# Performance work log

Measured on AMD Instinct MI355X. Metric: run time of the kernel, lower is better.

## Reference

```python
import jax, jax.numpy as jnp
import numpy as np

N_ITEMS = 1_000_000
N_FACTORS = 64

def setup_inputs() -> dict:
    key = jax.random.key(0)
    emb_weight = jax.random.normal(key, (N_ITEMS, N_FACTORS), dtype=jnp.float32)
    return {"emb_weight": emb_weight, "item_idx": 12345, "size": 50}

def reference(emb_weight, item_idx, size):
    # gather query row: u = emb(ind)  -> [d]
    u = emb_weight[item_idx]
    # scores = u @ emb.T  -> [n_items] (GEMV against full table)
    scores = emb_weight @ u
    # top-k retrieval (size <= n_items, clamp as in original)
    k = min(size, scores.shape[0])
    s, i = jax.lax.top_k(scores, k)
    return s, i
```

## Files before the change

### kernel.cpp

```cpp
#include <hip/hip_runtime.h>

#define NEG_INF (-1.0e30f)
#define CAP 4096
#define NBKT 4096

__device__ __forceinline__ unsigned flip(float f) {
    unsigned u = __float_as_uint(f);
    return (u & 0x80000000u) ? ~u : (u | 0x80000000u);
}

__device__ __forceinline__ bool pair_gt(float sa, int ia, float sb, int ib) {
    return (sa > sb) || (sa == sb && ia < ib);
}

__global__ __launch_bounds__(256) void k_gemv(const float* __restrict__ emb,
                                              const int* __restrict__ p_idx,
                                              float* __restrict__ scores) {
    const int tid   = threadIdx.x;
    const int col16 = tid & 15;
    const int grp   = tid >> 4;
    const float4 u4 = ((const float4*)(emb + (size_t)(*p_idx) * 64))[col16];
    const int base  = blockIdx.x * 64;
#pragma unroll
    for (int sub = 0; sub < 4; ++sub) {
        const int item = base + sub * 16 + grp;
        const float4 r = ((const float4*)(emb + (size_t)item * 64))[col16];
        float p = r.x * u4.x + r.y * u4.y + r.z * u4.z + r.w * u4.w;
        p += __shfl_xor(p, 1, 16);
        p += __shfl_xor(p, 2, 16);
        p += __shfl_xor(p, 4, 16);
        p += __shfl_xor(p, 8, 16);
        if (col16 == 0) scores[item] = p;
    }
}

__global__ __launch_bounds__(256) void k_hist(const float* __restrict__ scores,
                                              int n4, unsigned* __restrict__ hist) {
    __shared__ unsigned h[NBKT];
    const int tid = threadIdx.x;
    for (int i = tid; i < NBKT; i += 256) h[i] = 0;
    __syncthreads();
    const float4* s4 = (const float4*)scores;
    for (int i = blockIdx.x * 256 + tid; i < n4; i += gridDim.x * 256) {
        float4 v = s4[i];
        atomicAdd(&h[flip(v.x) >> 20], 1u);
        atomicAdd(&h[flip(v.y) >> 20], 1u);
        atomicAdd(&h[flip(v.z) >> 20], 1u);
        atomicAdd(&h[flip(v.w) >> 20], 1u);
    }
    __syncthreads();
    for (int i = tid; i < NBKT; i += 256) {
        unsigned c = h[i];
        if (c) atomicAdd(&hist[i], c);
    }
}

__global__ __launch_bounds__(256) void k_pick(const unsigned* __restrict__ hist,
                                              int k, unsigned* __restrict__ params) {
    __shared__ unsigned h[NBKT];
    __shared__ unsigned psum[256];
    const int tid = threadIdx.x;
    for (int i = tid; i < NBKT; i += 256) h[i] = hist[i];
    __syncthreads();
    const int base = tid * 16;
    unsigned local = 0;
#pragma unroll
    for (int j = 0; j < 16; ++j) local += h[base + j];
    psum[tid] = local;
    __syncthreads();
    for (int stride = 1; stride < 256; stride <<= 1) {
        unsigned add = (tid + stride < 256) ? psum[tid + stride] : 0u;
        __syncthreads();
        psum[tid] += add;
        __syncthreads();
    }
    unsigned c = (tid + 1 < 256) ? psum[tid + 1] : 0u;
    int found_b = -1; unsigned found_above = 0;
    for (int j = 15; j >= 0; --j) {
        unsigned hb = h[base + j];
        if (c < (unsigned)k && c + hb >= (unsigned)k) { found_b = base + j; found_above = c; }
        c += hb;
    }
    if (found_b >= 0) { params[0] = (unsigned)found_b; params[1] = found_above; }
}

__global__ __launch_bounds__(256) void k_compact(const float* __restrict__ scores,
                                                 int n4,
                                                 const unsigned* __restrict__ params,
                                                 unsigned* __restrict__ cnt,
                                                 float* __restrict__ cand_s,
                                                 int* __restrict__ cand_i) {
    const unsigned B = params[0];
    const float4* s4 = (const float4*)scores;
    for (int i = blockIdx.x * 256 + threadIdx.x; i < n4; i += gridDim.x * 256) {
        float4 v = s4[i];
        const float vv[4] = {v.x, v.y, v.z, v.w};
#pragma unroll
        for (int j = 0; j < 4; ++j) {
            if ((flip(vv[j]) >> 20) >= B) {
                unsigned pos = atomicAdd(cnt, 1u);
                if (pos < CAP) { cand_s[pos] = vv[j]; cand_i[pos] = i * 4 + j; }
            }
        }
    }
}

__global__ __launch_bounds__(256) void k_final(const float* __restrict__ cand_s,
                                               const int* __restrict__ cand_i,
                                               const unsigned* __restrict__ cnt,
                                               int k, float* __restrict__ out) {
    __shared__ float ss[CAP];
    __shared__ int   si[CAP];
    const int tid = threadIdx.x;
    unsigned c = *cnt;
    const int n = (c > CAP) ? CAP : (int)c;
    int N = 64; while (N < n) N <<= 1;
    for (int i = tid; i < N; i += 256) {
        const bool v = i < n;
        ss[i] = v ? cand_s[i] : NEG_INF;
        si[i] = v ? cand_i[i] : 0x7fffffff;
    }
    __syncthreads();
    for (int kk = 2; kk <= N; kk <<= 1) {
        for (int j = kk >> 1; j > 0; j >>= 1) {
            for (int i = tid; i < N; i += 256) {
                int l = i ^ j;
                if (l > i) {
                    float s_i = ss[i], s_l = ss[l];
                    int   d_i = si[i], d_l = si[l];
                    bool sw = ((i & kk) == 0) ? pair_gt(s_l, d_l, s_i, d_i)
                                              : pair_gt(s_i, d_i, s_l, d_l);
                    if (sw) { ss[i] = s_l; si[i] = d_l; ss[l] = s_i; si[l] = d_i; }
                }
            }
            __syncthreads();
        }
    }
    if (tid < k) {
        out[tid]     = ss[tid];
        out[k + tid] = (float)si[tid];
    }
}

extern "C" void kernel_launch(void* const* d_in, const int* in_sizes, int n_in,
                              void* d_out, int out_size, void* d_ws, size_t ws_size,
                              hipStream_t stream) {
    const float* emb   = (const float*)d_in[0];
    const int*   p_idx = (const int*)d_in[1];
    const int n_items  = in_sizes[0] / 64;
    const int k        = out_size / 2;

    float*    scores = (float*)d_ws;
    unsigned* hist   = (unsigned*)(scores + n_items);
    unsigned* params = hist + NBKT;
    unsigned* cnt    = params + 2;
    float*    cand_s = (float*)(cnt + 1);
    int*      cand_i = (int*)(cand_s + CAP);

    hipMemsetAsync(hist, 0, (NBKT + 3) * sizeof(unsigned), stream);

    const int n4 = n_items / 4;
    k_gemv   <<<n_items / 64, 256, 0, stream>>>(emb, p_idx, scores);
    k_hist   <<<128, 256, 0, stream>>>(scores, n4, hist);
    k_pick   <<<1,   256, 0, stream>>>(hist, k, params);
    k_compact<<<128, 256, 0, stream>>>(scores, n4, params, cnt, cand_s, cand_i);
    k_final  <<<1,   256, 0, stream>>>(cand_s, cand_i, cnt, k, (float*)d_out);
}
```

Baseline: 368.5 us.

## Restructure GEMV to 4 lanes per row and fuse threshold pick into compact

The GEMV kernel now gives each row to 4 lanes that each load four float4s, with every thread handling two rows. This cuts the shuffle reduction to two steps and raises the number of bytes in flight per thread. The single-block pick kernel is removed: each compact block redundantly rebuilds the prefix sum over the histogram in shared memory to find the threshold bucket, saving one launch at the cost of repeated 16KB histogram reads in every block.

```diff
diff --git a/kernel.cpp b/kernel.cpp
--- a/kernel.cpp
+++ b/kernel.cpp
@@ -15,22 +15,44 @@
 
 __global__ __launch_bounds__(256) void k_gemv(const float* __restrict__ emb,
                                               const int* __restrict__ p_idx,
+                                              int n_items,
                                               float* __restrict__ scores) {
     const int tid   = threadIdx.x;
-    const int col16 = tid & 15;
-    const int grp   = tid >> 4;
-    const float4 u4 = ((const float4*)(emb + (size_t)(*p_idx) * 64))[col16];
-    const int base  = blockIdx.x * 64;
-#pragma unroll
-    for (int sub = 0; sub < 4; ++sub) {
-        const int item = base + sub * 16 + grp;
-        const float4 r = ((const float4*)(emb + (size_t)item * 64))[col16];
-        float p = r.x * u4.x + r.y * u4.y + r.z * u4.z + r.w * u4.w;
-        p += __shfl_xor(p, 1, 16);
-        p += __shfl_xor(p, 2, 16);
-        p += __shfl_xor(p, 4, 16);
-        p += __shfl_xor(p, 8, 16);
-        if (col16 == 0) scores[item] = p;
+    const int lane4 = tid & 3;
+    const int rowg  = tid >> 2;
+    const float4* up = (const float4*)(emb + (size_t)(*p_idx) * 64);
+    const float4 u0 = up[lane4];
+    const float4 u1 = up[lane4 + 4];
+    const float4 u2 = up[lane4 + 8];
+    const float4 u3 = up[lane4 + 12];
+
+    const int item_a = blockIdx.x * 128 + rowg;
+    const int item_b = item_a + 64;
+
+    float pa = NEG_INF, pb = NEG_INF;
+    if (item_a < n_items) {
+        const float4* rp = (const float4*)(emb + (size_t)item_a * 64);
+        const float4 v0 = rp[lane4], v1 = rp[lane4 + 4], v2 = rp[lane4 + 8], v3 = rp[lane4 + 12];
+        float q0 = v0.x*u0.x + v0.y*u0.y + v0.z*u0.z + v0.w*u0.w;
+        float q1 = v1.x*u1.x + v1.y*u1.y + v1.z*u1.z + v1.w*u1.w;
+        float q2 = v2.x*u2.x + v2.y*u2.y + v2.z*u2.z + v2.w*u2.w;
+        float q3 = v3.x*u3.x + v3.y*u3.y + v3.z*u3.z + v3.w*u3.w;
+        pa = (q0 + q1) + (q2 + q3);
+    }
+    if (item_b < n_items) {
+        const float4* rp = (const float4*)(emb + (size_t)item_b * 64);
+        const float4 v0 = rp[lane4], v1 = rp[lane4 + 4], v2 = rp[lane4 + 8], v3 = rp[lane4 + 12];
+        float q0 = v0.x*u0.x + v0.y*u0.y + v0.z*u0.z + v0.w*u0.w;
+        float q1 = v1.x*u1.x + v1.y*u1.y + v1.z*u1.z + v1.w*u1.w;
+        float q2 = v2.x*u2.x + v2.y*u2.y + v2.z*u2.z + v2.w*u2.w;
+        float q3 = v3.x*u3.x + v3.y*u3.y + v3.z*u3.z + v3.w*u3.w;
+        pb = (q0 + q1) + (q2 + q3);
+    }
+    pa += __shfl_xor(pa, 1, 4);  pa += __shfl_xor(pa, 2, 4);
+    pb += __shfl_xor(pb, 1, 4);  pb += __shfl_xor(pb, 2, 4);
+    if (lane4 == 0) {
+        if (item_a < n_items) scores[item_a] = pa;
+        if (item_b < n_items) scores[item_b] = pb;
     }
 }
 
@@ -55,10 +77,16 @@
     }
 }
 
-__global__ __launch_bounds__(256) void k_pick(const unsigned* __restrict__ hist,
-                                              int k, unsigned* __restrict__ params) {
+__global__ __launch_bounds__(256) void k_compact(const float* __restrict__ scores,
+                                                 int n4,
+                                                 const unsigned* __restrict__ hist,
+                                                 int k,
+                                                 unsigned* __restrict__ cnt,
+                                                 float* __restrict__ cand_s,
+                                                 int* __restrict__ cand_i) {
     __shared__ unsigned h[NBKT];
     __shared__ unsigned psum[256];
+    __shared__ unsigned sB;
     const int tid = threadIdx.x;
     for (int i = tid; i < NBKT; i += 256) h[i] = hist[i];
     __syncthreads();
@@ -75,24 +103,16 @@
         __syncthreads();
     }
     unsigned c = (tid + 1 < 256) ? psum[tid + 1] : 0u;
-    int found_b = -1; unsigned found_above = 0;
     for (int j = 15; j >= 0; --j) {
         unsigned hb = h[base + j];
-        if (c < (unsigned)k && c + hb >= (unsigned)k) { found_b = base + j; found_above = c; }
+        if (c < (unsigned)k && c + hb >= (unsigned)k) sB = (unsigned)(base + j);
         c += hb;
     }
-    if (found_b >= 0) { params[0] = (unsigned)found_b; params[1] = found_above; }
-}
+    __syncthreads();
+    const unsigned B = sB;
 
-__global__ __launch_bounds__(256) void k_compact(const float* __restrict__ scores,
-                                                 int n4,
-                                                 const unsigned* __restrict__ params,
-                                                 unsigned* __restrict__ cnt,
-                                                 float* __restrict__ cand_s,
-                                                 int* __restrict__ cand_i) {
-    const unsigned B = params[0];
     const float4* s4 = (const float4*)scores;
-    for (int i = blockIdx.x * 256 + threadIdx.x; i < n4; i += gridDim.x * 256) {
+    for (int i = blockIdx.x * 256 + tid; i < n4; i += gridDim.x * 256) {
         float4 v = s4[i];
         const float vv[4] = {v.x, v.y, v.z, v.w};
 #pragma unroll
@@ -152,17 +172,16 @@
 
     float*    scores = (float*)d_ws;
     unsigned* hist   = (unsigned*)(scores + n_items);
-    unsigned* params = hist + NBKT;
-    unsigned* cnt    = params + 2;
+    unsigned* cnt    = hist + NBKT;
     float*    cand_s = (float*)(cnt + 1);
     int*      cand_i = (int*)(cand_s + CAP);
 
-    hipMemsetAsync(hist, 0, (NBKT + 3) * sizeof(unsigned), stream);
+    hipMemsetAsync(hist, 0, (NBKT + 1) * sizeof(unsigned), stream);
 
     const int n4 = n_items / 4;
-    k_gemv   <<<n_items / 64, 256, 0, stream>>>(emb, p_idx, scores);
+    const int g1 = (n_items + 127) / 128;
+    k_gemv   <<<g1,  256, 0, stream>>>(emb, p_idx, n_items, scores);
     k_hist   <<<128, 256, 0, stream>>>(scores, n4, hist);
-    k_pick   <<<1,   256, 0, stream>>>(hist, k, params);
-    k_compact<<<128, 256, 0, stream>>>(scores, n4, params, cnt, cand_s, cand_i);
+    k_compact<<<128, 256, 0, stream>>>(scores, n4, hist, k, cnt, cand_s, cand_i);
     k_final  <<<1,   256, 0, stream>>>(cand_s, cand_i, cnt, k, (float*)d_out);
 }
```

Measured after the change: 370.3 us. About the same (+0.5%).

## Fuse GEMV with histogram and threshold pick with compaction

Applied to the files above, without the earlier changes.

Scores are computed one row per thread with the query held in registers, and each score goes straight into the shared-memory histogram, removing a separate pass over the scores array and a kernel launch. The threshold bucket selection is now recomputed inside every compaction block instead of in a separate single-block kernel. The trade-off is a lane-strided row access pattern that may coalesce worse, plus redundant per-block scan work.

```diff
diff --git a/kernel.cpp b/kernel.cpp
--- a/kernel.cpp
+++ b/kernel.cpp
@@ -13,52 +13,51 @@
     return (sa > sb) || (sa == sb && ia < ib);
 }
 
-__global__ __launch_bounds__(256) void k_gemv(const float* __restrict__ emb,
-                                              const int* __restrict__ p_idx,
-                                              float* __restrict__ scores) {
-    const int tid   = threadIdx.x;
-    const int col16 = tid & 15;
-    const int grp   = tid >> 4;
-    const float4 u4 = ((const float4*)(emb + (size_t)(*p_idx) * 64))[col16];
-    const int base  = blockIdx.x * 64;
-#pragma unroll
-    for (int sub = 0; sub < 4; ++sub) {
-        const int item = base + sub * 16 + grp;
-        const float4 r = ((const float4*)(emb + (size_t)item * 64))[col16];
-        float p = r.x * u4.x + r.y * u4.y + r.z * u4.z + r.w * u4.w;
-        p += __shfl_xor(p, 1, 16);
-        p += __shfl_xor(p, 2, 16);
-        p += __shfl_xor(p, 4, 16);
-        p += __shfl_xor(p, 8, 16);
-        if (col16 == 0) scores[item] = p;
-    }
-}
-
-__global__ __launch_bounds__(256) void k_hist(const float* __restrict__ scores,
-                                              int n4, unsigned* __restrict__ hist) {
+__global__ __launch_bounds__(256) void k_gemv_hist(const float* __restrict__ emb,
+                                                   const int* __restrict__ p_idx,
+                                                   int n_items,
+                                                   float* __restrict__ scores,
+                                                   unsigned* __restrict__ hist) {
     __shared__ unsigned h[NBKT];
     const int tid = threadIdx.x;
     for (int i = tid; i < NBKT; i += 256) h[i] = 0;
+
+    const float4* uq = (const float4*)(emb + (size_t)(*p_idx) * 64);
+    float4 u[16];
+#pragma unroll
+    for (int c = 0; c < 16; ++c) u[c] = uq[c];
     __syncthreads();
-    const float4* s4 = (const float4*)scores;
-    for (int i = blockIdx.x * 256 + tid; i < n4; i += gridDim.x * 256) {
-        float4 v = s4[i];
-        atomicAdd(&h[flip(v.x) >> 20], 1u);
-        atomicAdd(&h[flip(v.y) >> 20], 1u);
-        atomicAdd(&h[flip(v.z) >> 20], 1u);
-        atomicAdd(&h[flip(v.w) >> 20], 1u);
+
+    const int stride = gridDim.x * 256;
+    for (int row = blockIdx.x * 256 + tid; row < n_items; row += stride) {
+        const float4* rp = (const float4*)(emb + (size_t)row * 64);
+        float acc = 0.0f;
+#pragma unroll
+        for (int c = 0; c < 16; ++c) {
+            const float4 r = rp[c];
+            acc += r.x * u[c].x + r.y * u[c].y + r.z * u[c].z + r.w * u[c].w;
+        }
+        scores[row] = acc;
+        atomicAdd(&h[flip(acc) >> 20], 1u);
     }
+
     __syncthreads();
     for (int i = tid; i < NBKT; i += 256) {
-        unsigned c = h[i];
+        const unsigned c = h[i];
         if (c) atomicAdd(&hist[i], c);
     }
 }
 
-__global__ __launch_bounds__(256) void k_pick(const unsigned* __restrict__ hist,
-                                              int k, unsigned* __restrict__ params) {
+__global__ __launch_bounds__(256) void k_compact(const float* __restrict__ scores,
+                                                 int n4,
+                                                 const unsigned* __restrict__ hist,
+                                                 int k,
+                                                 unsigned* __restrict__ cnt,
+                                                 float* __restrict__ cand_s,
+                                                 int* __restrict__ cand_i) {
     __shared__ unsigned h[NBKT];
     __shared__ unsigned psum[256];
+    __shared__ unsigned sB;
     const int tid = threadIdx.x;
     for (int i = tid; i < NBKT; i += 256) h[i] = hist[i];
     __syncthreads();
@@ -75,24 +74,16 @@
         __syncthreads();
     }
     unsigned c = (tid + 1 < 256) ? psum[tid + 1] : 0u;
-    int found_b = -1; unsigned found_above = 0;
     for (int j = 15; j >= 0; --j) {
         unsigned hb = h[base + j];
-        if (c < (unsigned)k && c + hb >= (unsigned)k) { found_b = base + j; found_above = c; }
+        if (c < (unsigned)k && c + hb >= (unsigned)k) sB = (unsigned)(base + j);
         c += hb;
     }
-    if (found_b >= 0) { params[0] = (unsigned)found_b; params[1] = found_above; }
-}
+    __syncthreads();
+    const unsigned B = sB;
 
-__global__ __launch_bounds__(256) void k_compact(const float* __restrict__ scores,
-                                                 int n4,
-                                                 const unsigned* __restrict__ params,
-                                                 unsigned* __restrict__ cnt,
-                                                 float* __restrict__ cand_s,
-                                                 int* __restrict__ cand_i) {
-    const unsigned B = params[0];
     const float4* s4 = (const float4*)scores;
-    for (int i = blockIdx.x * 256 + threadIdx.x; i < n4; i += gridDim.x * 256) {
+    for (int i = blockIdx.x * 256 + tid; i < n4; i += gridDim.x * 256) {
         float4 v = s4[i];
         const float vv[4] = {v.x, v.y, v.z, v.w};
 #pragma unroll
@@ -152,17 +143,14 @@
 
     float*    scores = (float*)d_ws;
     unsigned* hist   = (unsigned*)(scores + n_items);
-    unsigned* params = hist + NBKT;
-    unsigned* cnt    = params + 2;
+    unsigned* cnt    = hist + NBKT;
     float*    cand_s = (float*)(cnt + 1);
     int*      cand_i = (int*)(cand_s + CAP);
 
-    hipMemsetAsync(hist, 0, (NBKT + 3) * sizeof(unsigned), stream);
+    hipMemsetAsync(hist, 0, (NBKT + 1) * sizeof(unsigned), stream);
 
     const int n4 = n_items / 4;
-    k_gemv   <<<n_items / 64, 256, 0, stream>>>(emb, p_idx, scores);
-    k_hist   <<<128, 256, 0, stream>>>(scores, n4, hist);
-    k_pick   <<<1,   256, 0, stream>>>(hist, k, params);
-    k_compact<<<128, 256, 0, stream>>>(scores, n4, params, cnt, cand_s, cand_i);
-    k_final  <<<1,   256, 0, stream>>>(cand_s, cand_i, cnt, k, (float*)d_out);
+    k_gemv_hist<<<1024, 256, 0, stream>>>(emb, p_idx, n_items, scores, hist);
+    k_compact  <<<256,  256, 0, stream>>>(scores, n4, hist, k, cnt, cand_s, cand_i);
+    k_final    <<<1,    256, 0, stream>>>(cand_s, cand_i, cnt, k, (float*)d_out);
 }
```

Result: no change. 370.5 us (+0.6%).
